# Performance work log

Measured on AMD Instinct MI355X. Metric: run time of the kernel, lower is better.

The kernel has to match this reference:

```python
import jax, jax.numpy as jnp
import numpy as np

K = 2  # number of propagation hops (init arg k)


def setup_inputs() -> dict:
    key = jax.random.key(0)
    k1, k2, k3 = jax.random.split(key, 3)
    N, E, D = 100000, 1200000, 64
    feat = jax.random.normal(k1, (N, D), dtype=jnp.float32)
    src = jax.random.randint(k2, (E,), 0, N, dtype=jnp.int32)
    dst = jax.random.randint(k3, (E,), 0, N, dtype=jnp.int32)
    return {"feat": feat, "src": src, "dst": dst, "n_nodes": N}


def reference(feat, src, dst, n_nodes):
    # in-degree normalization: norm = clamp(in_deg, 1)^-0.5, shape [N, 1]
    deg = jax.ops.segment_sum(
        jnp.ones(dst.shape, dtype=feat.dtype), dst, num_segments=n_nodes
    )
    norm = jnp.power(jnp.maximum(deg, 1.0), -0.5)[:, None]
    for _ in range(K):
        feat = feat * norm                      # pre-scale by D^-1/2
        msgs = feat[src]                        # copy_u: gather source features [E, D]
        feat = jax.ops.segment_sum(msgs, dst, num_segments=n_nodes)  # sum at dst
        feat = feat * norm                      # post-scale by D^-1/2
    return feat
```

## Files before the change

### kernel.cpp

```cpp
#include <hip/hip_runtime.h>
#include <hip/hip_fp16.h>

#define D 64
#define BSH2 8
#define NPB 256
#define NB2_MAX 512
#define PCHUNK 4096
#define CAPP 6144
#define CAP2 4096


__global__ void zero_f32(float* __restrict__ p, long n) {
    long i = (long)blockIdx.x * blockDim.x + threadIdx.x;
    long stride = (long)gridDim.x * blockDim.x;
    for (; i < n; i += stride) p[i] = 0.0f;
}

__global__ void init_cursors(int* __restrict__ gcur, int NB2) {
    int i = blockIdx.x * blockDim.x + threadIdx.x;
    if (i < NB2) gcur[i << 4] = i * CAPP;
}

__global__ __launch_bounds__(256) void feat_to_half(const float4* __restrict__ in,
                                                    const float* __restrict__ norm,
                                                    uint2* __restrict__ out, long n4) {
    long i = (long)blockIdx.x * blockDim.x + threadIdx.x;
    if (i < n4) {
        float4 v = in[i];
        float r = norm[i >> 4];
        __half2 a = __floats2half2_rn(v.x * r, v.y * r);
        __half2 b = __floats2half2_rn(v.z * r, v.w * r);
        uint2 u;
        u.x = *(unsigned int*)&a;
        u.y = *(unsigned int*)&b;
        out[i] = u;
    }
}

__global__ __launch_bounds__(1024) void partition_direct(const int* __restrict__ src,
                                                         const int* __restrict__ dst,
                                                         int* __restrict__ gcur,
                                                         int* __restrict__ packed,
                                                         int E, int NB2) {
    __shared__ int staged[PCHUNK];
    __shared__ int lhist[NB2_MAX];
    __shared__ int lbase[NB2_MAX];
    __shared__ int lcur[NB2_MAX];
    __shared__ int gbase[NB2_MAX];
    int tid = threadIdx.x;
    int c0 = blockIdx.x * PCHUNK;
    int c1 = c0 + PCHUNK; if (c1 > E) c1 = E;

    if (tid < NB2_MAX) lhist[tid] = 0;
    __syncthreads();

    for (int e = c0 + tid * 4; e + 4 <= c1; e += 4096) {
        int4 d4 = *(const int4*)(dst + e);
        atomicAdd(&lhist[d4.x >> BSH2], 1);
        atomicAdd(&lhist[d4.y >> BSH2], 1);
        atomicAdd(&lhist[d4.z >> BSH2], 1);
        atomicAdd(&lhist[d4.w >> BSH2], 1);
    }
    int tail = c0 + ((c1 - c0) & ~3);
    for (int e = tail + tid; e < c1; e += 1024)
        atomicAdd(&lhist[dst[e] >> BSH2], 1);
    __syncthreads();

    if (tid < 64) {
        const int CPL = NB2_MAX / 64;
        int tmp[CPL];
        int s = 0;
        int base = tid * CPL;
        #pragma unroll
        for (int j = 0; j < CPL; j++) { tmp[j] = s; s += lhist[base + j]; }
        int incl = s;
        #pragma unroll
        for (int o = 1; o < 64; o <<= 1) {
            int t = __shfl_up(incl, o, 64);
            if (tid >= o) incl += t;
        }
        int excl = incl - s;
        #pragma unroll
        for (int j = 0; j < CPL; j++) {
            lbase[base + j] = excl + tmp[j];
            lcur[base + j]  = excl + tmp[j];
        }
    }
    __syncthreads();

    for (int e = c0 + tid * 4; e + 4 <= c1; e += 4096) {
        int4 d4 = *(const int4*)(dst + e);
        int4 s4 = *(const int4*)(src + e);
        int k, pos;
        k = d4.x >> BSH2; pos = atomicAdd(&lcur[k], 1);
        staged[pos] = s4.x | ((d4.x & (NPB - 1)) << 20);
        k = d4.y >> BSH2; pos = atomicAdd(&lcur[k], 1);
        staged[pos] = s4.y | ((d4.y & (NPB - 1)) << 20);
        k = d4.z >> BSH2; pos = atomicAdd(&lcur[k], 1);
        staged[pos] = s4.z | ((d4.z & (NPB - 1)) << 20);
        k = d4.w >> BSH2; pos = atomicAdd(&lcur[k], 1);
        staged[pos] = s4.w | ((d4.w & (NPB - 1)) << 20);
    }
    for (int e = tail + tid; e < c1; e += 1024) {
        int d = dst[e];
        int k = d >> BSH2;
        int pos = atomicAdd(&lcur[k], 1);
        staged[pos] = src[e] | ((d & (NPB - 1)) << 20);
    }
    __syncthreads();

    if (tid < NB2_MAX && tid < NB2) {
        int c = lhist[tid];
        gbase[tid] = c ? atomicAdd(&gcur[tid << 4], (c + 15) & ~15) : 0;
    }
    __syncthreads();

    int grp = tid >> 4, sub = tid & 15;
    for (int k = grp; k < NB2; k += 64) {
        int c = lhist[k];
        if (!c) continue;
        int c16 = (c + 15) & ~15;
        int g = gbase[k], base = lbase[k];
        for (int i = sub; i < c16; i += 16)
            packed[g + i] = (i < c) ? staged[base + i] : -1;
    }
}

__global__ __launch_bounds__(1024) void bucket_csr(const int* __restrict__ packed,
                                                   const int* __restrict__ gcur,
                                                   int2* __restrict__ rbc,
                                                   float* __restrict__ norm,
                                                   float* __restrict__ norm2,
                                                   int* __restrict__ csr,
                                                   int N, int NB2) {
    __shared__ int cnt[NPB];
    __shared__ int loc[NPB];
    int b = blockIdx.x;
    int tid = threadIdx.x;
    if (tid < NPB) cnt[tid] = 0;
    __syncthreads();

    int rbeg = b * CAPP;
    int rend = gcur[b << 4];
    for (int e = rbeg + tid * 4; e + 4 <= rend; e += 4096) {
        int4 p4 = *(const int4*)(packed + e);
        if (p4.x != -1) atomicAdd(&cnt[(p4.x >> 20) & (NPB - 1)], 1);
        if (p4.y != -1) atomicAdd(&cnt[(p4.y >> 20) & (NPB - 1)], 1);
        if (p4.z != -1) atomicAdd(&cnt[(p4.z >> 20) & (NPB - 1)], 1);
        if (p4.w != -1) atomicAdd(&cnt[(p4.w >> 20) & (NPB - 1)], 1);
    }
    __syncthreads();
    if (tid < 64) {
        int tmp[4];
        int s = 0;
        int base = tid * 4;
        #pragma unroll
        for (int j = 0; j < 4; j++) { tmp[j] = s; s += cnt[base + j]; }
        int incl = s;
        #pragma unroll
        for (int o = 1; o < 64; o <<= 1) {
            int t = __shfl_up(incl, o, 64);
            if (tid >= o) incl += t;
        }
        int excl = incl - s;
        #pragma unroll
        for (int j = 0; j < 4; j++) loc[base + j] = excl + tmp[j];
    }
    __syncthreads();

    int cbase = b * CAP2;
    if (tid < NPB) {
        int node = (b << BSH2) + tid;
        if (node < N) {
            int v = cnt[tid];
            int ep = loc[tid];
            rbc[node] = make_int2(cbase + ep, v);
            float df = (float)v; df = df < 1.0f ? 1.0f : df;
            float r = rsqrtf(df);
            norm[node] = r;
            norm2[node] = r * r;
        }
    }
    __syncthreads();
    for (int e = rbeg + tid * 4; e + 4 <= rend; e += 4096) {
        int4 p4 = *(const int4*)(packed + e);
        int l, pos;
        if (p4.x != -1) { l = (p4.x >> 20) & (NPB - 1); pos = atomicAdd(&loc[l], 1); csr[cbase + pos] = p4.x & 0xFFFFF; }
        if (p4.y != -1) { l = (p4.y >> 20) & (NPB - 1); pos = atomicAdd(&loc[l], 1); csr[cbase + pos] = p4.y & 0xFFFFF; }
        if (p4.z != -1) { l = (p4.z >> 20) & (NPB - 1); pos = atomicAdd(&loc[l], 1); csr[cbase + pos] = p4.z & 0xFFFFF; }
        if (p4.w != -1) { l = (p4.w >> 20) & (NPB - 1); pos = atomicAdd(&loc[l], 1); csr[cbase + pos] = p4.w & 0xFFFFF; }
    }
}

template <bool OUTHALF>
__global__ __launch_bounds__(256) void gather_h(const __half* __restrict__ x,
                                                const int2* __restrict__ rbc,
                                                const int* __restrict__ csr,
                                                const float* __restrict__ post,
                                                void* __restrict__ outv, int N) {
    int w = blockIdx.x * 4 + (threadIdx.x >> 6);
    if (w >= N) return;
    int lane = threadIdx.x & 63;
    int g = lane >> 3;
    int sub = lane & 7;
    int2 bc = rbc[w];
    int beg = bc.x, end = bc.x + bc.y;
    const uint4* x16 = (const uint4*)x;
    float a[8];
    #pragma unroll
    for (int i = 0; i < 8; i++) a[i] = 0.f;
    int e = beg + g;
    for (; e + 8 < end; e += 16) {
        int s0 = csr[e];
        int s1 = csr[e + 8];
        uint4 u0 = x16[s0 * 8 + sub];
        uint4 u1 = x16[s1 * 8 + sub];
        float2 f;
        f = __half22float2(*(const __half2*)&u0.x); a[0] += f.x; a[1] += f.y;
        f = __half22float2(*(const __half2*)&u0.y); a[2] += f.x; a[3] += f.y;
        f = __half22float2(*(const __half2*)&u0.z); a[4] += f.x; a[5] += f.y;
        f = __half22float2(*(const __half2*)&u0.w); a[6] += f.x; a[7] += f.y;
        f = __half22float2(*(const __half2*)&u1.x); a[0] += f.x; a[1] += f.y;
        f = __half22float2(*(const __half2*)&u1.y); a[2] += f.x; a[3] += f.y;
        f = __half22float2(*(const __half2*)&u1.z); a[4] += f.x; a[5] += f.y;
        f = __half22float2(*(const __half2*)&u1.w); a[6] += f.x; a[7] += f.y;
    }
    if (e < end) {
        int s0 = csr[e];
        uint4 u0 = x16[s0 * 8 + sub];
        float2 f;
        f = __half22float2(*(const __half2*)&u0.x); a[0] += f.x; a[1] += f.y;
        f = __half22float2(*(const __half2*)&u0.y); a[2] += f.x; a[3] += f.y;
        f = __half22float2(*(const __half2*)&u0.z); a[4] += f.x; a[5] += f.y;
        f = __half22float2(*(const __half2*)&u0.w); a[6] += f.x; a[7] += f.y;
    }
    #pragma unroll
    for (int i = 0; i < 8; i++) {
        a[i] += __shfl_xor(a[i], 8, 64);
        a[i] += __shfl_xor(a[i], 16, 64);
        a[i] += __shfl_xor(a[i], 32, 64);
    }
    if (g == 0) {
        float pn = post[w];
        #pragma unroll
        for (int i = 0; i < 8; i++) a[i] *= pn;
        if (OUTHALF) {
            __half2 h0 = __floats2half2_rn(a[0], a[1]);
            __half2 h1 = __floats2half2_rn(a[2], a[3]);
            __half2 h2 = __floats2half2_rn(a[4], a[5]);
            __half2 h3 = __floats2half2_rn(a[6], a[7]);
            uint4 u;
            u.x = *(unsigned int*)&h0;
            u.y = *(unsigned int*)&h1;
            u.z = *(unsigned int*)&h2;
            u.w = *(unsigned int*)&h3;
            ((uint4*)outv)[(long)w * 8 + sub] = u;
        } else {
            float4 r0; r0.x = a[0]; r0.y = a[1]; r0.z = a[2]; r0.w = a[3];
            float4 r1; r1.x = a[4]; r1.y = a[5]; r1.z = a[6]; r1.w = a[7];
            ((float4*)outv)[(long)w * 16 + sub * 2]     = r0;
            ((float4*)outv)[(long)w * 16 + sub * 2 + 1] = r1;
        }
    }
}


__global__ void deg_kernel_f(const int* __restrict__ dst, float* __restrict__ deg, int E) {
    int e = blockIdx.x * blockDim.x + threadIdx.x;
    if (e < E) unsafeAtomicAdd(&deg[dst[e]], 1.0f);
}

__global__ void norm_kernel_f(float* __restrict__ deg_norm, float* __restrict__ norm2, int N) {
    int i = blockIdx.x * blockDim.x + threadIdx.x;
    if (i < N) {
        float d = deg_norm[i];
        d = d < 1.0f ? 1.0f : d;
        float r = rsqrtf(d);
        deg_norm[i] = r;
        norm2[i] = r * r;
    }
}

__global__ void scatter_kernel(const float* __restrict__ x,
                               const float* __restrict__ scale,
                               const int* __restrict__ src,
                               const int* __restrict__ dst,
                               float* __restrict__ out, int E) {
    long idx = (long)blockIdx.x * blockDim.x + threadIdx.x;
    int e = (int)(idx >> 6);
    int lane = (int)(idx & 63);
    if (e < E) {
        int s = src[e];
        int d0 = dst[e];
        float v = x[(long)s * D + lane] * scale[s];
        unsafeAtomicAdd(&out[(long)d0 * D + lane], v);
    }
}

__global__ void scale_kernel(float* __restrict__ out, const float* __restrict__ norm, long n) {
    long i = (long)blockIdx.x * blockDim.x + threadIdx.x;
    if (i < n) out[i] *= norm[i >> 6];
}


extern "C" void kernel_launch(void* const* d_in, const int* in_sizes, int n_in,
                              void* d_out, int out_size, void* d_ws, size_t ws_size,
                              hipStream_t stream) {
    const float* feat = (const float*)d_in[0];
    const int*   src  = (const int*)d_in[1];
    const int*   dst  = (const int*)d_in[2];
    float* out = (float*)d_out;

    const int N = in_sizes[0] / D;
    const int E = in_sizes[1];
    const long ND = (long)N * D;
    const int NB2 = (N + NPB - 1) >> BSH2;

    long o_gcur = 0;
    long o_rbc  = o_gcur + NB2_MAX * 16;
    long o_norm = o_rbc + 2L * N;
    long o_norm2 = o_norm + N;
    long o_csr  = (o_norm2 + N + 3) & ~3L;
    long o_f16  = (o_csr + (long)NB2 * CAP2 + 3) & ~3L;
    long o_buf1 = (o_f16 + ND / 2 + 3) & ~3L;
    long pk_len = (long)NB2 * CAPP;
    long buf1_len = (ND / 2 > pk_len) ? ND / 2 : pk_len;
    size_t need = (size_t)(o_buf1 + buf1_len) * 4;

    if (ws_size >= need && N <= (1 << 20) && NB2 <= NB2_MAX) {
        int*   bi = (int*)d_ws;
        float* bf = (float*)d_ws;
        int* gcur    = bi + o_gcur;
        int2* rbc    = (int2*)(bi + o_rbc);
        float* norm  = bf + o_norm;
        float* norm2 = bf + o_norm2;
        int* csr     = bi + o_csr;
        __half* feat16 = (__half*)(bi + o_f16);
        __half* buf1h  = (__half*)(bi + o_buf1);
        int* packed  = bi + o_buf1;

        int pblocks = (E + PCHUNK - 1) / PCHUNK;

        init_cursors<<<(NB2 + 255) / 256, 256, 0, stream>>>(gcur, NB2);
        partition_direct<<<pblocks, 1024, 0, stream>>>(src, dst, gcur, packed, E, NB2);
        bucket_csr<<<NB2, 1024, 0, stream>>>(packed, gcur, rbc, norm, norm2, csr, N, NB2);
        long n4 = ND / 4;
        feat_to_half<<<(int)((n4 + 255) / 256), 256, 0, stream>>>(
            (const float4*)feat, norm, (uint2*)feat16, n4);

        int gblocks = (N + 3) / 4;
        gather_h<true><<<gblocks, 256, 0, stream>>>(feat16, rbc, csr, norm2, buf1h, N);
        gather_h<false><<<gblocks, 256, 0, stream>>>(buf1h, rbc, csr, norm, out, N);
    } else {
        float* norm  = (float*)d_ws;
        float* norm2 = norm + N;
        float* buf1  = norm2 + N;

        long nz = 2L * N + ND;
        zero_f32<<<(int)((nz + 255) / 256), 256, 0, stream>>>((float*)d_ws, nz);
        zero_f32<<<(int)((ND + 255) / 256), 256, 0, stream>>>(out, ND);
        deg_kernel_f<<<(E + 255) / 256, 256, 0, stream>>>(dst, norm, E);
        norm_kernel_f<<<(N + 255) / 256, 256, 0, stream>>>(norm, norm2, N);
        long work = (long)E * D;
        int blocks = (int)((work + 255) / 256);
        scatter_kernel<<<blocks, 256, 0, stream>>>(feat, norm, src, dst, buf1, E);
        scatter_kernel<<<blocks, 256, 0, stream>>>(buf1, norm2, src, dst, out, E);
        scale_kernel<<<(int)((ND + 255) / 256), 256, 0, stream>>>(out, norm, ND);
    }
}
```

Before: 184.5 us.

## Split half-precision features into four column quarters for cache-friendlier gathers

Features are stored in half precision as four separate column quarters (16 channels each), and the gather kernels process one quarter per block range with 32 lanes per node. Each quarter is only a quarter the size of the full table, so the randomly gathered working set is more likely to stay in L2/LLC, while edge indices are re-read four times. The intra-wave reduction and the output indexing are rewritten for the new lane mapping.

```diff
diff --git a/kernel.cpp b/kernel.cpp
--- a/kernel.cpp
+++ b/kernel.cpp
@@ -21,19 +21,23 @@
     if (i < NB2) gcur[i << 4] = i * CAPP;
 }
 
-__global__ __launch_bounds__(256) void feat_to_half(const float4* __restrict__ in,
-                                                    const float* __restrict__ norm,
-                                                    uint2* __restrict__ out, long n4) {
+__global__ __launch_bounds__(256) void feat_to_half_q(const float4* __restrict__ in,
+                                                      const float* __restrict__ norm,
+                                                      uint2* __restrict__ out, int N) {
     long i = (long)blockIdx.x * blockDim.x + threadIdx.x;
+    long n4 = (long)N * 16;
     if (i < n4) {
         float4 v = in[i];
-        float r = norm[i >> 4];
+        int node = (int)(i >> 4);
+        int t = (int)(i & 15);
+        int q = t >> 2, j = t & 3;
+        float r = norm[node];
         __half2 a = __floats2half2_rn(v.x * r, v.y * r);
         __half2 b = __floats2half2_rn(v.z * r, v.w * r);
         uint2 u;
         u.x = *(unsigned int*)&a;
         u.y = *(unsigned int*)&b;
-        out[i] = u;
+        out[(long)q * N * 4 + node * 4 + j] = u;
     }
 }
 
@@ -193,28 +197,34 @@
 }
 
 template <bool OUTHALF>
-__global__ __launch_bounds__(256) void gather_h(const __half* __restrict__ x,
+__global__ __launch_bounds__(256) void gather_q(const __half* __restrict__ xq,
                                                 const int2* __restrict__ rbc,
                                                 const int* __restrict__ csr,
                                                 const float* __restrict__ post,
-                                                void* __restrict__ outv, int N) {
-    int w = blockIdx.x * 4 + (threadIdx.x >> 6);
+                                                void* __restrict__ outv,
+                                                int N, int nbq) {
+    int q = blockIdx.x / nbq;
+    int b = blockIdx.x - q * nbq;
+    int wv = threadIdx.x >> 6;
+    int lane = threadIdx.x & 63;
+    int half32 = lane >> 5;
+    int l32 = lane & 31;
+    int w = b * 8 + wv * 2 + half32;
     if (w >= N) return;
-    int lane = threadIdx.x & 63;
-    int g = lane >> 3;
-    int sub = lane & 7;
+    int g = l32 >> 1;
+    int sub = l32 & 1;
     int2 bc = rbc[w];
     int beg = bc.x, end = bc.x + bc.y;
-    const uint4* x16 = (const uint4*)x;
+    const uint4* x16 = ((const uint4*)xq) + (long)q * N * 2;
     float a[8];
     #pragma unroll
     for (int i = 0; i < 8; i++) a[i] = 0.f;
     int e = beg + g;
-    for (; e + 8 < end; e += 16) {
+    for (; e + 16 < end; e += 32) {
         int s0 = csr[e];
-        int s1 = csr[e + 8];
-        uint4 u0 = x16[s0 * 8 + sub];
-        uint4 u1 = x16[s1 * 8 + sub];
+        int s1 = csr[e + 16];
+        uint4 u0 = x16[s0 * 2 + sub];
+        uint4 u1 = x16[s1 * 2 + sub];
         float2 f;
         f = __half22float2(*(const __half2*)&u0.x); a[0] += f.x; a[1] += f.y;
         f = __half22float2(*(const __half2*)&u0.y); a[2] += f.x; a[3] += f.y;
@@ -227,7 +237,7 @@
     }
     if (e < end) {
         int s0 = csr[e];
-        uint4 u0 = x16[s0 * 8 + sub];
+        uint4 u0 = x16[s0 * 2 + sub];
         float2 f;
         f = __half22float2(*(const __half2*)&u0.x); a[0] += f.x; a[1] += f.y;
         f = __half22float2(*(const __half2*)&u0.y); a[2] += f.x; a[3] += f.y;
@@ -236,9 +246,10 @@
     }
     #pragma unroll
     for (int i = 0; i < 8; i++) {
+        a[i] += __shfl_xor(a[i], 2, 64);
+        a[i] += __shfl_xor(a[i], 4, 64);
         a[i] += __shfl_xor(a[i], 8, 64);
         a[i] += __shfl_xor(a[i], 16, 64);
-        a[i] += __shfl_xor(a[i], 32, 64);
     }
     if (g == 0) {
         float pn = post[w];
@@ -254,12 +265,12 @@
             u.y = *(unsigned int*)&h1;
             u.z = *(unsigned int*)&h2;
             u.w = *(unsigned int*)&h3;
-            ((uint4*)outv)[(long)w * 8 + sub] = u;
+            ((uint4*)outv)[(long)q * N * 2 + (long)w * 2 + sub] = u;
         } else {
             float4 r0; r0.x = a[0]; r0.y = a[1]; r0.z = a[2]; r0.w = a[3];
             float4 r1; r1.x = a[4]; r1.y = a[5]; r1.z = a[6]; r1.w = a[7];
-            ((float4*)outv)[(long)w * 16 + sub * 2]     = r0;
-            ((float4*)outv)[(long)w * 16 + sub * 2 + 1] = r1;
+            ((float4*)outv)[(long)w * 16 + q * 4 + sub * 2]     = r0;
+            ((float4*)outv)[(long)w * 16 + q * 4 + sub * 2 + 1] = r1;
         }
     }
 }
@@ -345,12 +356,12 @@
         partition_direct<<<pblocks, 1024, 0, stream>>>(src, dst, gcur, packed, E, NB2);
         bucket_csr<<<NB2, 1024, 0, stream>>>(packed, gcur, rbc, norm, norm2, csr, N, NB2);
         long n4 = ND / 4;
-        feat_to_half<<<(int)((n4 + 255) / 256), 256, 0, stream>>>(
-            (const float4*)feat, norm, (uint2*)feat16, n4);
-
-        int gblocks = (N + 3) / 4;
-        gather_h<true><<<gblocks, 256, 0, stream>>>(feat16, rbc, csr, norm2, buf1h, N);
-        gather_h<false><<<gblocks, 256, 0, stream>>>(buf1h, rbc, csr, norm, out, N);
+        feat_to_half_q<<<(int)((n4 + 255) / 256), 256, 0, stream>>>(
+            (const float4*)feat, norm, (uint2*)feat16, N);
+
+        int nbq = (N + 7) / 8;
+        gather_q<true><<<nbq * 4, 256, 0, stream>>>(feat16, rbc, csr, norm2, buf1h, N, nbq);
+        gather_q<false><<<nbq * 4, 256, 0, stream>>>(buf1h, rbc, csr, norm, out, N, nbq);
     } else {
         float* norm  = (float*)d_ws;
         float* norm2 = norm + N;
```

New measurement: 246.7 us. +33.7%, slower.

## Fuse fp16 feature conversion into bucket_csr and batch gather loads by degree

Applied to the files above, without the earlier changes.

Drops the separate feat_to_half kernel: each bucket_csr block now scales its own 256 nodes' features by the inverse-sqrt degree from its local count and writes them as fp16. The gather kernel is restructured into degree-specialised bursts that issue all csr index loads and then all feature loads before accumulating, using masked multiplies instead of branches to raise memory-level parallelism. The final fp32 output uses nontemporal stores. This removes one launch and one pass over the features, at the cost of more wasted masked loads on low-degree rows and more register pressure.

```diff
diff --git a/kernel.cpp b/kernel.cpp
--- a/kernel.cpp
+++ b/kernel.cpp
@@ -9,6 +9,8 @@
 #define CAPP 6144
 #define CAP2 4096
 
+typedef float f32x4 __attribute__((ext_vector_type(4)));
+
 
 __global__ void zero_f32(float* __restrict__ p, long n) {
     long i = (long)blockIdx.x * blockDim.x + threadIdx.x;
@@ -19,22 +21,6 @@
 __global__ void init_cursors(int* __restrict__ gcur, int NB2) {
     int i = blockIdx.x * blockDim.x + threadIdx.x;
     if (i < NB2) gcur[i << 4] = i * CAPP;
-}
-
-__global__ __launch_bounds__(256) void feat_to_half(const float4* __restrict__ in,
-                                                    const float* __restrict__ norm,
-                                                    uint2* __restrict__ out, long n4) {
-    long i = (long)blockIdx.x * blockDim.x + threadIdx.x;
-    if (i < n4) {
-        float4 v = in[i];
-        float r = norm[i >> 4];
-        __half2 a = __floats2half2_rn(v.x * r, v.y * r);
-        __half2 b = __floats2half2_rn(v.z * r, v.w * r);
-        uint2 u;
-        u.x = *(unsigned int*)&a;
-        u.y = *(unsigned int*)&b;
-        out[i] = u;
-    }
 }
 
 __global__ __launch_bounds__(1024) void partition_direct(const int* __restrict__ src,
@@ -132,6 +118,8 @@
                                                    float* __restrict__ norm,
                                                    float* __restrict__ norm2,
                                                    int* __restrict__ csr,
+                                                   const float4* __restrict__ feat,
+                                                   uint2* __restrict__ fq,
                                                    int N, int NB2) {
     __shared__ int cnt[NPB];
     __shared__ int loc[NPB];
@@ -190,50 +178,86 @@
         if (p4.z != -1) { l = (p4.z >> 20) & (NPB - 1); pos = atomicAdd(&loc[l], 1); csr[cbase + pos] = p4.z & 0xFFFFF; }
         if (p4.w != -1) { l = (p4.w >> 20) & (NPB - 1); pos = atomicAdd(&loc[l], 1); csr[cbase + pos] = p4.w & 0xFFFFF; }
     }
+
+    #pragma unroll
+    for (int it = 0; it < 4; it++) {
+        int item = tid + it * 1024;
+        int l = item >> 4;
+        int node = (b << BSH2) + l;
+        if (node < N) {
+            int t = item & 15;
+            float4 v = feat[(long)node * 16 + t];
+            float df = (float)cnt[l]; df = df < 1.0f ? 1.0f : df;
+            float r = rsqrtf(df);
+            __half2 a = __floats2half2_rn(v.x * r, v.y * r);
+            __half2 bb = __floats2half2_rn(v.z * r, v.w * r);
+            uint2 u;
+            u.x = *(unsigned int*)&a;
+            u.y = *(unsigned int*)&bb;
+            fq[(long)node * 16 + t] = u;
+        }
+    }
+}
+
+template <int NS>
+__device__ __forceinline__ void burst(const uint4* __restrict__ x16,
+                                      const int* __restrict__ csr,
+                                      int beg, int deg, int off,
+                                      int g, int sub, float* a) {
+    int e[NS]; float m[NS]; int s[NS]; uint4 u[NS];
+    #pragma unroll
+    for (int i = 0; i < NS; i++) {
+        int idx = g + off + 8 * i;
+        bool v = idx < deg;
+        e[i] = v ? beg + idx : beg;
+        m[i] = v ? 1.f : 0.f;
+    }
+    #pragma unroll
+    for (int i = 0; i < NS; i++) s[i] = csr[e[i]];
+    #pragma unroll
+    for (int i = 0; i < NS; i++) u[i] = x16[s[i] * 8 + sub];
+    #pragma unroll
+    for (int i = 0; i < NS; i++) {
+        float2 f;
+        f = __half22float2(*(const __half2*)&u[i].x); a[0] += f.x * m[i]; a[1] += f.y * m[i];
+        f = __half22float2(*(const __half2*)&u[i].y); a[2] += f.x * m[i]; a[3] += f.y * m[i];
+        f = __half22float2(*(const __half2*)&u[i].z); a[4] += f.x * m[i]; a[5] += f.y * m[i];
+        f = __half22float2(*(const __half2*)&u[i].w); a[6] += f.x * m[i]; a[7] += f.y * m[i];
+    }
 }
 
 template <bool OUTHALF>
-__global__ __launch_bounds__(256) void gather_h(const __half* __restrict__ x,
-                                                const int2* __restrict__ rbc,
-                                                const int* __restrict__ csr,
-                                                const float* __restrict__ post,
-                                                void* __restrict__ outv, int N) {
+__global__ __launch_bounds__(256) void gather_row(const __half* __restrict__ x,
+                                                  const int2* __restrict__ rbc,
+                                                  const int* __restrict__ csr,
+                                                  const float* __restrict__ post,
+                                                  void* __restrict__ outv, int N) {
     int w = blockIdx.x * 4 + (threadIdx.x >> 6);
     if (w >= N) return;
     int lane = threadIdx.x & 63;
     int g = lane >> 3;
     int sub = lane & 7;
     int2 bc = rbc[w];
-    int beg = bc.x, end = bc.x + bc.y;
+    int beg = bc.x, deg = bc.y;
     const uint4* x16 = (const uint4*)x;
+    float pn = post[w];
     float a[8];
     #pragma unroll
     for (int i = 0; i < 8; i++) a[i] = 0.f;
-    int e = beg + g;
-    for (; e + 8 < end; e += 16) {
-        int s0 = csr[e];
-        int s1 = csr[e + 8];
-        uint4 u0 = x16[s0 * 8 + sub];
-        uint4 u1 = x16[s1 * 8 + sub];
-        float2 f;
-        f = __half22float2(*(const __half2*)&u0.x); a[0] += f.x; a[1] += f.y;
-        f = __half22float2(*(const __half2*)&u0.y); a[2] += f.x; a[3] += f.y;
-        f = __half22float2(*(const __half2*)&u0.z); a[4] += f.x; a[5] += f.y;
-        f = __half22float2(*(const __half2*)&u0.w); a[6] += f.x; a[7] += f.y;
-        f = __half22float2(*(const __half2*)&u1.x); a[0] += f.x; a[1] += f.y;
-        f = __half22float2(*(const __half2*)&u1.y); a[2] += f.x; a[3] += f.y;
-        f = __half22float2(*(const __half2*)&u1.z); a[4] += f.x; a[5] += f.y;
-        f = __half22float2(*(const __half2*)&u1.w); a[6] += f.x; a[7] += f.y;
-    }
-    if (e < end) {
-        int s0 = csr[e];
-        uint4 u0 = x16[s0 * 8 + sub];
-        float2 f;
-        f = __half22float2(*(const __half2*)&u0.x); a[0] += f.x; a[1] += f.y;
-        f = __half22float2(*(const __half2*)&u0.y); a[2] += f.x; a[3] += f.y;
-        f = __half22float2(*(const __half2*)&u0.z); a[4] += f.x; a[5] += f.y;
-        f = __half22float2(*(const __half2*)&u0.w); a[6] += f.x; a[7] += f.y;
-    }
+
+    if (deg > 0) {
+        if (deg <= 8) {
+            burst<1>(x16, csr, beg, deg, 0, g, sub, a);
+        } else if (deg <= 16) {
+            burst<2>(x16, csr, beg, deg, 0, g, sub, a);
+        } else if (deg <= 32) {
+            burst<4>(x16, csr, beg, deg, 0, g, sub, a);
+        } else {
+            for (int off = 0; off < deg; off += 32)
+                burst<4>(x16, csr, beg, deg, off, g, sub, a);
+        }
+    }
+
     #pragma unroll
     for (int i = 0; i < 8; i++) {
         a[i] += __shfl_xor(a[i], 8, 64);
@@ -241,7 +265,6 @@
         a[i] += __shfl_xor(a[i], 32, 64);
     }
     if (g == 0) {
-        float pn = post[w];
         #pragma unroll
         for (int i = 0; i < 8; i++) a[i] *= pn;
         if (OUTHALF) {
@@ -256,10 +279,10 @@
             u.w = *(unsigned int*)&h3;
             ((uint4*)outv)[(long)w * 8 + sub] = u;
         } else {
-            float4 r0; r0.x = a[0]; r0.y = a[1]; r0.z = a[2]; r0.w = a[3];
-            float4 r1; r1.x = a[4]; r1.y = a[5]; r1.z = a[6]; r1.w = a[7];
-            ((float4*)outv)[(long)w * 16 + sub * 2]     = r0;
-            ((float4*)outv)[(long)w * 16 + sub * 2 + 1] = r1;
+            f32x4 r0; r0.x = a[0]; r0.y = a[1]; r0.z = a[2]; r0.w = a[3];
+            f32x4 r1; r1.x = a[4]; r1.y = a[5]; r1.z = a[6]; r1.w = a[7];
+            __builtin_nontemporal_store(r0, ((f32x4*)outv) + (long)w * 16 + sub * 2);
+            __builtin_nontemporal_store(r1, ((f32x4*)outv) + (long)w * 16 + sub * 2 + 1);
         }
     }
 }
@@ -343,14 +366,12 @@
 
         init_cursors<<<(NB2 + 255) / 256, 256, 0, stream>>>(gcur, NB2);
         partition_direct<<<pblocks, 1024, 0, stream>>>(src, dst, gcur, packed, E, NB2);
-        bucket_csr<<<NB2, 1024, 0, stream>>>(packed, gcur, rbc, norm, norm2, csr, N, NB2);
-        long n4 = ND / 4;
-        feat_to_half<<<(int)((n4 + 255) / 256), 256, 0, stream>>>(
-            (const float4*)feat, norm, (uint2*)feat16, n4);
+        bucket_csr<<<NB2, 1024, 0, stream>>>(packed, gcur, rbc, norm, norm2, csr,
+                                             (const float4*)feat, (uint2*)feat16, N, NB2);
 
         int gblocks = (N + 3) / 4;
-        gather_h<true><<<gblocks, 256, 0, stream>>>(feat16, rbc, csr, norm2, buf1h, N);
-        gather_h<false><<<gblocks, 256, 0, stream>>>(buf1h, rbc, csr, norm, out, N);
+        gather_row<true><<<gblocks, 256, 0, stream>>>(feat16, rbc, csr, norm2, buf1h, N);
+        gather_row<false><<<gblocks, 256, 0, stream>>>(buf1h, rbc, csr, norm, out, N);
     } else {
         float* norm  = (float*)d_ws;
         float* norm2 = norm + N;
```

Result: faster. 171.0 us (-7.3%).
